# Kernel tuning notes

Hardware: AMD Instinct MI355X
Metric: run time of the kernel (lower is better)

The kernel has to match this reference:

```python
import jax, jax.numpy as jnp
import numpy as np

N = 100000
E = 1600000
D = 128          # in_feat == hidden_size
L = 3            # hidden layers
EPS = 1e-5       # BatchNorm1d eps


def setup_inputs() -> dict:
    key = jax.random.key(0)
    ks = jax.random.split(key, 12)
    x = jax.random.normal(ks[0], (N, D), dtype=jnp.float32)
    edge_index = jax.random.randint(ks[1], (2, E), 0, N, dtype=jnp.int64)
    s = 1.0 / np.sqrt(D)
    # stacked hidden-layer SAGEConv params: lin_l (neighbor), lin_r (root), bias on lin_l
    Wl = jax.random.uniform(ks[2], (L, D, D), jnp.float32, -s, s)
    Wr = jax.random.uniform(ks[3], (L, D, D), jnp.float32, -s, s)
    b = jax.random.uniform(ks[4], (L, D), jnp.float32, -s, s)
    # batchnorm affine params
    gamma = jnp.ones((L, D), jnp.float32)
    beta = jnp.zeros((L, D), jnp.float32)
    # output SAGEConv: D -> 1
    Wl_out = jax.random.uniform(ks[5], (D, 1), jnp.float32, -s, s)
    Wr_out = jax.random.uniform(ks[6], (D, 1), jnp.float32, -s, s)
    b_out = jax.random.uniform(ks[7], (1,), jnp.float32, -s, s)
    return {"x": x, "edge_index": edge_index, "Wl": Wl, "Wr": Wr, "b": b,
            "gamma": gamma, "beta": beta, "Wl_out": Wl_out, "Wr_out": Wr_out,
            "b_out": b_out}


def _sage(x, src, dst, inv_deg, Wl, Wr, b):
    # gather neighbor features along edges, mean-aggregate at destination
    msg_sum = jax.ops.segment_sum(x[src], dst, num_segments=N)   # [N, F]
    mean = msg_sum * inv_deg                                     # 0 for isolated nodes
    return mean @ Wl + x @ Wr + b


def _batchnorm(x, gamma, beta):
    m = jnp.mean(x, axis=0)
    v = jnp.mean((x - m) ** 2, axis=0)  # biased var, as torch BN uses for normalization
    return gamma * (x - m) * jax.lax.rsqrt(v + EPS) + beta


def reference(x, edge_index, Wl, Wr, b, gamma, beta, Wl_out, Wr_out, b_out):
    src, dst = edge_index[0], edge_index[1]
    deg = jax.ops.segment_sum(jnp.ones((E,), x.dtype), dst, num_segments=N)
    inv_deg = jnp.where(deg > 0, 1.0 / jnp.maximum(deg, 1.0), 0.0)[:, None]
    h = x
    for i in range(L):
        h = _sage(h, src, dst, inv_deg, Wl[i], Wr[i], b[i])
        h = jax.nn.relu(h)
        h = _batchnorm(h, gamma[i], beta[i])
    out = _sage(h, src, dst, inv_deg, Wl_out, Wr_out, b_out)
    return jax.nn.sigmoid(out)  # [N, 1]
```

## Files before the change

kernel.cpp:

```cpp
#include <hip/hip_runtime.h>

typedef unsigned short u16;
typedef unsigned int u32;
typedef unsigned long long u64;

#define GN 100000
#define GE 1600000
#define DCAP 64
#define NRANGE 196
#define NBKT (NRANGE * 8)
#define BCAP 1536

typedef __bf16 bf16x8 __attribute__((ext_vector_type(8)));
typedef float f32x4 __attribute__((ext_vector_type(4)));
typedef float f32x2 __attribute__((ext_vector_type(2)));
typedef u32 u32x4 __attribute__((ext_vector_type(4)));
typedef u32 u32x2 __attribute__((ext_vector_type(2)));

__device__ __forceinline__ float bl(u32 u){ return __uint_as_float(u << 16); }
__device__ __forceinline__ float bh(u32 u){ return __uint_as_float(u & 0xffff0000u); }
__device__ __forceinline__ float bfu(u16 v){ return __uint_as_float(((u32)v) << 16); }
__device__ __forceinline__ u16 f2bf(float f){
    u32 u = __float_as_uint(f);
    u32 r = (u + 0x7fffu + ((u >> 16) & 1u)) >> 16;
    return (u16)r;
}
__device__ __forceinline__ u32 pack2(float a, float b){
    return (u32)f2bf(a) | ((u32)f2bf(b) << 16);
}
__device__ __forceinline__ u32 pk8x4(float a, float b, float c, float d){
    u32 p = (u32)__builtin_amdgcn_cvt_pk_fp8_f32(a, b, 0, false);
    p = (u32)__builtin_amdgcn_cvt_pk_fp8_f32(c, d, p, true);
    return p;
}

__global__ void __launch_bounds__(256) k_init(const int* ei, const u32* xraw,
                                              int* cursor, float* colpart, int* flags,
                                              int* bcur){
    int i = blockIdx.x * 256 + threadIdx.x;
    if (i < GN) cursor[i] = 0;
    if (i < NBKT) bcur[i] = 0;
    if (i < 6144) colpart[i] = 0.f;
    int t = threadIdx.x;
    if (blockIdx.x == 0){
        __shared__ int s_any[4];
        int v = 0;
        #pragma unroll
        for (int j = 0; j < 4; ++j){
            int k = t * 4 + j;
            v |= ei[2 * k * 1000 + 1];
        }
        #pragma unroll
        for (int m = 1; m < 64; m <<= 1) v |= __shfl_xor(v, m);
        if ((t & 63) == 0) s_any[t >> 6] = v;
        __syncthreads();
        if (t == 0){
            int any = s_any[0] | s_any[1] | s_any[2] | s_any[3];
            flags[0] = (any == 0) ? 1 : 0;
        }
    }
    if (blockIdx.x == 1){
        __shared__ int s_cnt[4];
        int cnt = 0;
        #pragma unroll
        for (int j = 0; j < 4; ++j){
            int idx = (t * 4 + j) * 6000 + 3;
            u32 u = xraw[idx];
            int e = (u >> 7) & 0xFF;
            cnt += (e >= 100 && e <= 140) ? 1 : 0;
        }
        #pragma unroll
        for (int m = 1; m < 64; m <<= 1) cnt += __shfl_xor(cnt, m);
        if ((t & 63) == 0) s_cnt[t >> 6] = cnt;
        __syncthreads();
        if (t == 0){
            int tot = s_cnt[0] + s_cnt[1] + s_cnt[2] + s_cnt[3];
            flags[1] = (tot > 512) ? 0 : 1;
        }
    }
}

__global__ void __launch_bounds__(256) k_convx(const void* x, const int* flags,
                                               u16* xb, u32* h8){
    int gid = blockIdx.x * 256 + threadIdx.x;
    if (gid >= GN * 16) return;
    float f0,f1,f2,f3,f4,f5,f6,f7;
    if (flags[1]){
        const u32x4* xf = (const u32x4*)x;
        u32x4 a = __builtin_nontemporal_load(xf + gid * 2);
        u32x4 b = __builtin_nontemporal_load(xf + gid * 2 + 1);
        f0 = __uint_as_float(a.x); f1 = __uint_as_float(a.y);
        f2 = __uint_as_float(a.z); f3 = __uint_as_float(a.w);
        f4 = __uint_as_float(b.x); f5 = __uint_as_float(b.y);
        f6 = __uint_as_float(b.z); f7 = __uint_as_float(b.w);
    } else {
        u32x4 g = __builtin_nontemporal_load((const u32x4*)x + gid);
        f0 = bl(g.x); f1 = bh(g.x); f2 = bl(g.y); f3 = bh(g.y);
        f4 = bl(g.z); f5 = bh(g.z); f6 = bl(g.w); f7 = bh(g.w);
    }
    u32x4 o;
    o.x = pack2(f0, f1); o.y = pack2(f2, f3);
    o.z = pack2(f4, f5); o.w = pack2(f6, f7);
    ((u32x4*)xb)[gid] = o;
    u32x2 e = { pk8x4(f0, f1, f2, f3), pk8x4(f4, f5, f6, f7) };
    ((u32x2*)h8)[gid] = e;
}

__global__ void __launch_bounds__(256) k_tofp8(const u16* h, u32* h8){
    int gid = blockIdx.x * 256 + threadIdx.x;
    if (gid >= GN * 16) return;
    u32x4 g = ((const u32x4*)h)[gid];
    u32x2 e = { pk8x4(bl(g.x), bh(g.x), bl(g.y), bh(g.y)),
                pk8x4(bl(g.z), bh(g.z), bl(g.w), bh(g.w)) };
    ((u32x2*)h8)[gid] = e;
}

#define WOFF_WR    49152
#define WOFF_B     98304
#define WOFF_G     98688
#define WOFF_BE    99072
#define WOFF_WLO   99456
#define WOFF_WRO   99584
#define WOFF_BO    99712
#define WTOT       99713
__global__ void __launch_bounds__(256) k_convw(const void* Wl, const void* Wr, const void* b,
                                               const void* g, const void* be, const void* wlo,
                                               const void* wro, const void* bo,
                                               const int* flags, u16* wbuf, float* biasf){
    int i = blockIdx.x * 256 + threadIdx.x;
    if (i >= WTOT) return;
    const void* s; int k;
    if (i < WOFF_B){
        const void* src = (i < WOFF_WR) ? Wl : Wr;
        int r = (i < WOFF_WR) ? i : i - WOFF_WR;
        int layer = r >> 14, L = r & 16383;
        int kk = ((L >> 10) << 3) | (L & 7);
        int cc = (L >> 3) & 127;
        int si = layer * 16384 + kk * 128 + cc;
        float fv = flags[1] ? ((const float*)src)[si] : bfu(((const u16*)src)[si]);
        wbuf[i] = f2bf(fv);
        return;
    }
    if      (i < WOFF_G  ){ s = b;   k = i - WOFF_B; }
    else if (i < WOFF_BE ){ s = g;   k = i - WOFF_G; }
    else if (i < WOFF_WLO){ s = be;  k = i - WOFF_BE; }
    else if (i < WOFF_WRO){ s = wlo; k = i - WOFF_WLO; }
    else if (i < WOFF_BO ){ s = wro; k = i - WOFF_WRO; }
    else                  { s = bo;  k = 0; }
    float fv = flags[1] ? ((const float*)s)[k] : bfu(((const u16*)s)[k]);
    wbuf[i] = f2bf(fv);
    if (i >= WOFF_B && i < WOFF_B + 384) biasf[i - WOFF_B] = fv;
}

__global__ void __launch_bounds__(256) k_fillA(const int* ei, const int* flags,
                                               int* bcur, u64* pairs){
    __shared__ int cnt[256];
    __shared__ int lofs[256];
    __shared__ int gbase[NRANGE];
    __shared__ int wsum[4];
    __shared__ u64 lp[1024];
    int t = threadIdx.x;
    int lane = t & 63, w = t >> 6;
    int res = blockIdx.x & 7;
    int base = blockIdx.x * 1024;
    int is64 = flags[0];
    cnt[t] = 0;
    __syncthreads();
    int myd[4], mys[4], slot[4], myr[4];
    #pragma unroll
    for (int j = 0; j < 4; ++j){
        int e = base + j * 256 + t;
        if (e < GE){
            int d, s;
            if (is64){ d = __builtin_nontemporal_load(ei + 2 * (GE + e));
                       s = __builtin_nontemporal_load(ei + 2 * e); }
            else     { d = __builtin_nontemporal_load(ei + GE + e);
                       s = __builtin_nontemporal_load(ei + e); }
            myd[j] = d; mys[j] = s; myr[j] = d >> 9;
            slot[j] = atomicAdd(&cnt[myr[j]], 1);
        } else myr[j] = -1;
    }
    __syncthreads();
    int v = cnt[t];
    int sv = v;
    #pragma unroll
    for (int d = 1; d < 64; d <<= 1){
        int u = __shfl_up(sv, d);
        if (lane >= d) sv += u;
    }
    if (lane == 63) wsum[w] = sv;
    __syncthreads();
    int prefix = 0;
    #pragma unroll
    for (int j = 0; j < 4; ++j) if (j < w) prefix += wsum[j];
    lofs[t] = sv + prefix - v;
    if (t < NRANGE && cnt[t] > 0)
        gbase[t] = atomicAdd(&bcur[t * 8 + res], cnt[t]);
    __syncthreads();
    #pragma unroll
    for (int j = 0; j < 4; ++j){
        if (myr[j] >= 0)
            lp[lofs[myr[j]] + slot[j]] = ((u64)(u32)myd[j] << 32) | (u32)mys[j];
    }
    __syncthreads();
    int total = GE - base; if (total > 1024) total = 1024;
    for (int i = t; i < total; i += 256){
        u64 pr = lp[i];
        int r = (int)(pr >> 32) >> 9;
        int g = gbase[r] + (i - lofs[r]);
        if (g < BCAP) pairs[((size_t)(r * 8 + res)) * BCAP + g] = pr;
    }
}

__global__ void __launch_bounds__(256) k_fillB(const int* bcur, const u64* pairs,
                                               int* cursor, int* col){
    int range = blockIdx.x % 200;
    int sub   = blockIdx.x / 200;
    if (range >= NRANGE || sub >= 8) return;
    int bkt = range * 8 + sub;
    int n = bcur[bkt]; if (n > BCAP) n = BCAP;
    const u64* P = pairs + (size_t)bkt * BCAP;
    for (int i = threadIdx.x; i < n; i += 256){
        u64 pr = __builtin_nontemporal_load(P + i);
        int s = (int)(u32)pr, d = (int)(pr >> 32);
        int pos = atomicAdd(&cursor[d], 1);
        if (pos < DCAP) col[d * DCAP + pos] = s;
    }
}

__global__ void __launch_bounds__(256, 4) k_aggemm(const u32* h8, const int* deg, const int* col,
                                                   const u16* hin, const u16* Wlp, const u16* Wrp,
                                                   const float* biasf,
                                                   u16* hout, float* colpart){
    __shared__ __align__(16) u16 albuf[4][32][136];
    int t = threadIdx.x;
    int wid = t >> 6, lane = t & 63;
    int grp = lane >> 4, lg = lane & 15;
    int r0w = blockIdx.x * 128 + wid * 32;

    const u32x2* hrow = (const u32x2*)h8;
    #pragma unroll 1
    for (int round = 0; round < 8; ++round){
        int nl = round * 4 + grp;
        int node = r0w + nl;
        float a0=0.f,a1=0.f,a2=0.f,a3=0.f,a4=0.f,a5=0.f,a6=0.f,a7=0.f;
        if (node < GN){
            int d = deg[node];
            int cnt = d < DCAP ? d : DCAP;
            const int* nb = col + node * DCAP;
            int e = 0;
            #define ACC8(v) { \
                f32x2 d0 = __builtin_amdgcn_cvt_pk_f32_fp8((v).x, false); \
                f32x2 d1 = __builtin_amdgcn_cvt_pk_f32_fp8((v).x, true);  \
                f32x2 d2 = __builtin_amdgcn_cvt_pk_f32_fp8((v).y, false); \
                f32x2 d3 = __builtin_amdgcn_cvt_pk_f32_fp8((v).y, true);  \
                a0 += d0.x; a1 += d0.y; a2 += d1.x; a3 += d1.y;           \
                a4 += d2.x; a5 += d2.y; a6 += d3.x; a7 += d3.y; }
            for (; e + 7 < cnt; e += 8){
                u32x2 v0 = hrow[(size_t)nb[e]     * 16 + lg];
                u32x2 v1 = hrow[(size_t)nb[e + 1] * 16 + lg];
                u32x2 v2 = hrow[(size_t)nb[e + 2] * 16 + lg];
                u32x2 v3 = hrow[(size_t)nb[e + 3] * 16 + lg];
                u32x2 v4 = hrow[(size_t)nb[e + 4] * 16 + lg];
                u32x2 v5 = hrow[(size_t)nb[e + 5] * 16 + lg];
                u32x2 v6 = hrow[(size_t)nb[e + 6] * 16 + lg];
                u32x2 v7 = hrow[(size_t)nb[e + 7] * 16 + lg];
                ACC8(v0) ACC8(v1) ACC8(v2) ACC8(v3) ACC8(v4) ACC8(v5) ACC8(v6) ACC8(v7)
            }
            for (; e + 1 < cnt; e += 2){
                u32x2 v0 = hrow[(size_t)nb[e]     * 16 + lg];
                u32x2 v1 = hrow[(size_t)nb[e + 1] * 16 + lg];
                ACC8(v0) ACC8(v1)
            }
            if (e < cnt){
                u32x2 v0 = hrow[(size_t)nb[e] * 16 + lg];
                ACC8(v0)
            }
            #undef ACC8
            float inv = (d > 0) ? 1.f / (float)d : 0.f;
            a0*=inv; a1*=inv; a2*=inv; a3*=inv; a4*=inv; a5*=inv; a6*=inv; a7*=inv;
        }
        u32x4 o;
        o.x = pack2(a0, a1); o.y = pack2(a2, a3);
        o.z = pack2(a4, a5); o.w = pack2(a6, a7);
        *(u32x4*)(&albuf[wid][nl][lg * 8]) = o;
    }

    int quad = grp, l15 = lg;
    f32x4 acc[2][8];
    #pragma unroll
    for (int i = 0; i < 2; i++)
        #pragma unroll
        for (int j = 0; j < 8; j++) acc[i][j] = (f32x4){0.f, 0.f, 0.f, 0.f};

    #pragma unroll
    for (int half = 0; half < 2; ++half){
        const u16* W = half ? Wrp : Wlp;
        #pragma unroll
        for (int s = 0; s < 4; ++s){
            int kk = (s << 5) + (quad << 3);
            union { u32x4 u; bf16x8 v; } fn0, fn1;
            if (half == 0){
                fn0.u = *(const u32x4*)(&albuf[wid][l15][kk]);
                fn1.u = *(const u32x4*)(&albuf[wid][l15 + 16][kk]);
            } else {
                int n0 = r0w + l15, n1 = r0w + 16 + l15;
                fn0.u = (n0 < GN) ? *(const u32x4*)(hin + n0 * 128 + kk) : (u32x4){0,0,0,0};
                fn1.u = (n1 < GN) ? *(const u32x4*)(hin + n1 * 128 + kk) : (u32x4){0,0,0,0};
            }
            int kc = (s << 2) + quad;
            const u32x4* wg = (const u32x4*)W + (kc << 7) + l15;
            #pragma unroll
            for (int cb = 0; cb < 8; ++cb){
                union { u32x4 u; bf16x8 v; } fw;
                fw.u = wg[cb << 4];
                acc[0][cb] = __builtin_amdgcn_mfma_f32_16x16x32_bf16(fn0.v, fw.v, acc[0][cb], 0, 0, 0);
                acc[1][cb] = __builtin_amdgcn_mfma_f32_16x16x32_bf16(fn1.v, fw.v, acc[1][cb], 0, 0, 0);
            }
        }
    }

    __syncthreads();
    float* sst = (float*)albuf;
    sst[t] = 0.f;
    __syncthreads();

    int r0 = r0w;
    float bsv[8];
    #pragma unroll
    for (int cb = 0; cb < 8; cb++) bsv[cb] = biasf[cb * 16 + l15];

    #pragma unroll
    for (int cb = 0; cb < 8; cb++){
        float csum = 0.f, csq = 0.f;
        #pragma unroll
        for (int rb = 0; rb < 2; rb++){
            int rbase = r0 + rb * 16 + quad * 4;
            #pragma unroll
            for (int rr = 0; rr < 4; rr++){
                int row = rbase + rr;
                float v = acc[rb][cb][rr] + bsv[cb];
                v = fmaxf(v, 0.f);
                if (row < GN) hout[row * 128 + cb * 16 + l15] = f2bf(v);
                float vm = (row < GN) ? v : 0.f;
                csum += vm; csq += vm * vm;
            }
        }
        csum += __shfl_xor(csum, 16); csum += __shfl_xor(csum, 32);
        csq  += __shfl_xor(csq, 16);  csq  += __shfl_xor(csq, 32);
        if (quad == 0){
            atomicAdd(&sst[cb * 16 + l15], csum);
            atomicAdd(&sst[128 + cb * 16 + l15], csq);
        }
    }
    __syncthreads();
    atomicAdd(&colpart[(blockIdx.x & 7) * 256 + t], sst[t]);
}

__global__ void __launch_bounds__(256) k_bnf(const float* colpart, const u16* gamma, const u16* beta,
                                             int mode,
                                             const u16* WlN, const u16* WrN, u16* wfd,
                                             const float* bNsrc, float* bNdst,
                                             const u16* wlo, const u16* wro, const u16* bo,
                                             u16* hwl, u16* hwr, float* hb){
    __shared__ float s_sc[128], s_sh[128], s_red[256];
    int t = threadIdx.x, b = blockIdx.x;
    if (t < 128){
        float s = 0.f, q = 0.f;
        #pragma unroll
        for (int j = 0; j < 8; ++j){
            s += colpart[j * 256 + t];
            q += colpart[j * 256 + 128 + t];
        }
        const float invn = 1.f / (float)GN;
        float mean = s * invn;
        float var = fmaxf(q * invn - mean * mean, 0.f);
        float rstd = rsqrtf(var + 1e-5f);
        float g  = bfu(gamma[t]);
        float be = bfu(beta[t]);
        float sc = g * rstd, sh = be - mean * sc;
        s_sc[t] = sc; s_sh[t] = sh;
    }
    __syncthreads();
    if (mode == 0){
        if (b < 64){
            int idx = b * 256 + t;
            int k = ((idx >> 10) << 3) | (idx & 7);
            float sc = s_sc[k];
            wfd[idx]         = f2bf(sc * bfu(WlN[idx]));
            wfd[16384 + idx] = f2bf(sc * bfu(WrN[idx]));
        } else if (t < 128){
            float acc = bNsrc[t];
            for (int k = 0; k < 128; ++k){
                int L = ((k >> 3) << 10) + (t << 3) + (k & 7);
                acc += s_sh[k] * (bfu(WlN[L]) + bfu(WrN[L]));
            }
            bNdst[t] = acc;
        }
    } else if (b == 64){
        float contrib = 0.f;
        if (t < 128){
            float wl = bfu(wlo[t]), wr = bfu(wro[t]);
            hwl[t] = f2bf(s_sc[t] * wl);
            hwr[t] = f2bf(s_sc[t] * wr);
            contrib = s_sh[t] * (wl + wr);
        }
        s_red[t] = contrib;
        __syncthreads();
        for (int off = 128; off >= 1; off >>= 1){
            if (t < off) s_red[t] += s_red[t + off];
            __syncthreads();
        }
        if (t == 0) hb[0] = s_red[0] + bfu(bo[0]);
    }
}

__global__ void __launch_bounds__(256) k_dot(const u16* h, const u16* wl, const u16* wr,
                                             float* y, float* r){
    int node = (blockIdx.x * 256 + threadIdx.x) >> 6;
    int lane = threadIdx.x & 63;
    if (node >= GN) return;
    u32 hv  = ((const u32*)h)[node * 64 + lane];
    u32 wlv = ((const u32*)wl)[lane];
    u32 wrv = ((const u32*)wr)[lane];
    float hlo = bl(hv), hhi = bh(hv);
    float ya = hlo * bl(wlv) + hhi * bh(wlv);
    float ra = hlo * bl(wrv) + hhi * bh(wrv);
    #pragma unroll
    for (int m = 1; m < 64; m <<= 1){ ya += __shfl_xor(ya, m); ra += __shfl_xor(ra, m); }
    if (lane == 0){ y[node] = ya; r[node] = ra; }
}

__global__ void __launch_bounds__(256) k_out(const float* y, const float* r, const int* deg,
                                             const int* col, const float* hb,
                                             const int* flags, void* out){
    int n = blockIdx.x * 256 + threadIdx.x;
    if (n >= GN) return;
    int d = deg[n];
    int cnt = d < DCAP ? d : DCAP;
    const int* nb = col + n * DCAP;
    float s = 0.f;
    for (int e = 0; e < cnt; ++e) s += y[nb[e]];
    float inv = (d > 0) ? 1.f / (float)d : 0.f;
    float z = inv * s + r[n] + hb[0];
    float sg = 1.f / (1.f + __expf(-z));
    if (flags[1]) ((float*)out)[n] = sg;
    else          ((u16*)out)[n] = f2bf(sg);
}

extern "C" void kernel_launch(void* const* d_in, const int* in_sizes, int n_in,
                              void* d_out, int out_size, void* d_ws, size_t ws_size,
                              hipStream_t stream) {
    const void* x     = d_in[0];
    const int*  ei    = (const int*)d_in[1];
    const void* Wl    = d_in[2];
    const void* Wr    = d_in[3];
    const void* bias  = d_in[4];
    const void* gamma = d_in[5];
    const void* beta  = d_in[6];
    const void* wlout = d_in[7];
    const void* wrout = d_in[8];
    const void* bout  = d_in[9];

    char* p = (char*)d_ws;
    auto take = [&](size_t b){ void* q = (void*)p; p += (b + 255) & ~(size_t)255; return q; };
    int*   cursor = (int*)  take((size_t)GN * 4);
    int*   flags  = (int*)  take(256);
    int*   bcur   = (int*)  take((size_t)NBKT * 4);
    float* colpart= (float*)take(6144 * 4);
    float* biasf  = (float*)take(384 * 4);
    float* bf2    = (float*)take(128 * 4);
    float* bf3    = (float*)take(128 * 4);
    float* hb     = (float*)take(256);
    u16*   wf2    = (u16*)  take(32768 * 2);
    u16*   wf3    = (u16*)  take(32768 * 2);
    u16*   hwl    = (u16*)  take(128 * 2);
    u16*   hwr    = (u16*)  take(128 * 2);
    float* yv     = (float*)take((size_t)GN * 4);
    float* rv     = (float*)take((size_t)GN * 4);
    int*   col    = (int*)  take((size_t)GN * DCAP * 4);
    u16*   xb     = (u16*)  take((size_t)GN * 128 * 2);
    u16*   scrap  = (u16*)  take((size_t)GN * 128 * 2);
    u16*   hbuf   = (u16*)  take((size_t)GN * 128 * 2);
    u32*   h8     = (u32*)  take((size_t)GN * 128);
    u16*   wbuf   = (u16*)  take((size_t)WTOT * 2);

    u64* pairs = (u64*)scrap;

    const int NB_N = (GN + 255) / 256;
    const int NB_W = (GN + 3) / 4;
    const int NB_G = (GN + 127) / 128;
    const int NB_M = (GN * 16 + 255) / 256;
    const int NB_C = (WTOT + 255) / 256;
    const int NB_A = (GE + 1023) / 1024;

    k_init <<<NB_N, 256, 0, stream>>>(ei, (const u32*)x, cursor, colpart, flags, bcur);
    k_convx<<<NB_M, 256, 0, stream>>>(x, flags, xb, h8);
    k_convw<<<NB_C, 256, 0, stream>>>(Wl, Wr, bias, gamma, beta, wlout, wrout, bout, flags, wbuf, biasf);
    k_fillA<<<NB_A, 256, 0, stream>>>(ei, flags, bcur, pairs);
    k_fillB<<<1600, 256, 0, stream>>>(bcur, pairs, cursor, col);

    const u16* hin = xb;
    for (int i = 0; i < 3; ++i){
        const u16* Wlp; const u16* Wrp; const float* bfi;
        if (i == 0){ Wlp = wbuf;     Wrp = wbuf + WOFF_WR; bfi = biasf; }
        else if (i == 1){ Wlp = wf2; Wrp = wf2 + 16384;    bfi = bf2; }
        else { Wlp = wf3;            Wrp = wf3 + 16384;    bfi = bf3; }
        u16* wfd = (i == 0) ? wf2 : wf3;
        float* bNdst = (i == 0) ? bf2 : bf3;
        int nx = (i < 2) ? (i + 1) : 0;
        k_aggemm<<<NB_G, 256, 0, stream>>>(h8, cursor, col, hin, Wlp, Wrp, bfi, hbuf,
                                           colpart + i * 2048);
        k_bnf  <<<65, 256, 0, stream>>>(colpart + i * 2048,
            wbuf + WOFF_G + i * 128, wbuf + WOFF_BE + i * 128, (i == 2) ? 1 : 0,
            wbuf + nx * 16384, wbuf + WOFF_WR + nx * 16384, wfd,
            biasf + nx * 128, bNdst,
            wbuf + WOFF_WLO, wbuf + WOFF_WRO, wbuf + WOFF_BO, hwl, hwr, hb);
        if (i < 2) k_tofp8<<<NB_M, 256, 0, stream>>>(hbuf, h8);
        hin = hbuf;
    }
    k_dot<<<NB_W, 256, 0, stream>>>(hbuf, hwl, hwr, yv, rv);
    k_out<<<NB_N, 256, 0, stream>>>(yv, rv, cursor, col, hb, flags, d_out);
}
```

Measured before the change: 457.5 us.

## Split fused aggregate+GEMM kernel into separate gather and MFMA GEMM kernels

The fused per-layer kernel, which gathered fp8 neighbor rows into LDS and then ran the bf16 MFMA GEMM, is split into two kernels. A small 64-thread-block gather kernel writes bf16 mean rows to a global buffer, and a separate GEMM kernel reads them back. This aims to improve latency hiding and occupancy for the irregular gather by decoupling it from the register-heavy GEMM. The cost is an extra round trip of about 25.6 MB per layer through global memory, plus one more kernel launch per layer.

```diff
diff --git a/kernel.cpp b/kernel.cpp
--- a/kernel.cpp
+++ b/kernel.cpp
@@ -228,65 +228,68 @@
     }
 }
 
-__global__ void __launch_bounds__(256, 4) k_aggemm(const u32* h8, const int* deg, const int* col,
-                                                   const u16* hin, const u16* Wlp, const u16* Wrp,
-                                                   const float* biasf,
-                                                   u16* hout, float* colpart){
-    __shared__ __align__(16) u16 albuf[4][32][136];
+__global__ void __launch_bounds__(64) k_agg(const u32* h8, const int* deg, const int* col,
+                                            u16* amean){
+    int lane = threadIdx.x;
+    int grp = lane >> 4;
+    int lg  = lane & 15;
+    int node = blockIdx.x * 4 + grp;
+    if (node >= GN) return;
+    int d = deg[node];
+    int cnt = d < DCAP ? d : DCAP;
+    const int* nb = col + node * DCAP;
+    const u32x2* hrow = (const u32x2*)h8;
+    float a0=0.f,a1=0.f,a2=0.f,a3=0.f,a4=0.f,a5=0.f,a6=0.f,a7=0.f;
+    int e = 0;
+    #define ACC8(v) { \
+        f32x2 d0 = __builtin_amdgcn_cvt_pk_f32_fp8((v).x, false); \
+        f32x2 d1 = __builtin_amdgcn_cvt_pk_f32_fp8((v).x, true);  \
+        f32x2 d2 = __builtin_amdgcn_cvt_pk_f32_fp8((v).y, false); \
+        f32x2 d3 = __builtin_amdgcn_cvt_pk_f32_fp8((v).y, true);  \
+        a0 += d0.x; a1 += d0.y; a2 += d1.x; a3 += d1.y;           \
+        a4 += d2.x; a5 += d2.y; a6 += d3.x; a7 += d3.y; }
+    for (; e + 7 < cnt; e += 8){
+        u32x2 v0 = hrow[(size_t)nb[e]     * 16 + lg];
+        u32x2 v1 = hrow[(size_t)nb[e + 1] * 16 + lg];
+        u32x2 v2 = hrow[(size_t)nb[e + 2] * 16 + lg];
+        u32x2 v3 = hrow[(size_t)nb[e + 3] * 16 + lg];
+        u32x2 v4 = hrow[(size_t)nb[e + 4] * 16 + lg];
+        u32x2 v5 = hrow[(size_t)nb[e + 5] * 16 + lg];
+        u32x2 v6 = hrow[(size_t)nb[e + 6] * 16 + lg];
+        u32x2 v7 = hrow[(size_t)nb[e + 7] * 16 + lg];
+        ACC8(v0) ACC8(v1) ACC8(v2) ACC8(v3) ACC8(v4) ACC8(v5) ACC8(v6) ACC8(v7)
+    }
+    for (; e + 1 < cnt; e += 2){
+        u32x2 v0 = hrow[(size_t)nb[e]     * 16 + lg];
+        u32x2 v1 = hrow[(size_t)nb[e + 1] * 16 + lg];
+        ACC8(v0) ACC8(v1)
+    }
+    if (e < cnt){
+        u32x2 v0 = hrow[(size_t)nb[e] * 16 + lg];
+        ACC8(v0)
+    }
+    #undef ACC8
+    float inv = (d > 0) ? 1.f / (float)d : 0.f;
+    u32x4 o;
+    o.x = pack2(a0 * inv, a1 * inv);
+    o.y = pack2(a2 * inv, a3 * inv);
+    o.z = pack2(a4 * inv, a5 * inv);
+    o.w = pack2(a6 * inv, a7 * inv);
+    ((u32x4*)amean)[(size_t)node * 16 + lg] = o;
+}
+
+__global__ void __launch_bounds__(256, 4) k_gemm(const u16* amean, const u16* hin,
+                                                 const u16* Wlp, const u16* Wrp,
+                                                 const float* biasf,
+                                                 u16* hout, float* colpart){
+    __shared__ float sst[256];
     int t = threadIdx.x;
     int wid = t >> 6, lane = t & 63;
-    int grp = lane >> 4, lg = lane & 15;
-    int r0w = blockIdx.x * 128 + wid * 32;
-
-    const u32x2* hrow = (const u32x2*)h8;
-    #pragma unroll 1
-    for (int round = 0; round < 8; ++round){
-        int nl = round * 4 + grp;
-        int node = r0w + nl;
-        float a0=0.f,a1=0.f,a2=0.f,a3=0.f,a4=0.f,a5=0.f,a6=0.f,a7=0.f;
-        if (node < GN){
-            int d = deg[node];
-            int cnt = d < DCAP ? d : DCAP;
-            const int* nb = col + node * DCAP;
-            int e = 0;
-            #define ACC8(v) { \
-                f32x2 d0 = __builtin_amdgcn_cvt_pk_f32_fp8((v).x, false); \
-                f32x2 d1 = __builtin_amdgcn_cvt_pk_f32_fp8((v).x, true);  \
-                f32x2 d2 = __builtin_amdgcn_cvt_pk_f32_fp8((v).y, false); \
-                f32x2 d3 = __builtin_amdgcn_cvt_pk_f32_fp8((v).y, true);  \
-                a0 += d0.x; a1 += d0.y; a2 += d1.x; a3 += d1.y;           \
-                a4 += d2.x; a5 += d2.y; a6 += d3.x; a7 += d3.y; }
-            for (; e + 7 < cnt; e += 8){
-                u32x2 v0 = hrow[(size_t)nb[e]     * 16 + lg];
-                u32x2 v1 = hrow[(size_t)nb[e + 1] * 16 + lg];
-                u32x2 v2 = hrow[(size_t)nb[e + 2] * 16 + lg];
-                u32x2 v3 = hrow[(size_t)nb[e + 3] * 16 + lg];
-                u32x2 v4 = hrow[(size_t)nb[e + 4] * 16 + lg];
-                u32x2 v5 = hrow[(size_t)nb[e + 5] * 16 + lg];
-                u32x2 v6 = hrow[(size_t)nb[e + 6] * 16 + lg];
-                u32x2 v7 = hrow[(size_t)nb[e + 7] * 16 + lg];
-                ACC8(v0) ACC8(v1) ACC8(v2) ACC8(v3) ACC8(v4) ACC8(v5) ACC8(v6) ACC8(v7)
-            }
-            for (; e + 1 < cnt; e += 2){
-                u32x2 v0 = hrow[(size_t)nb[e]     * 16 + lg];
-                u32x2 v1 = hrow[(size_t)nb[e + 1] * 16 + lg];
-                ACC8(v0) ACC8(v1)
-            }
-            if (e < cnt){
-                u32x2 v0 = hrow[(size_t)nb[e] * 16 + lg];
-                ACC8(v0)
-            }
-            #undef ACC8
-            float inv = (d > 0) ? 1.f / (float)d : 0.f;
-            a0*=inv; a1*=inv; a2*=inv; a3*=inv; a4*=inv; a5*=inv; a6*=inv; a7*=inv;
-        }
-        u32x4 o;
-        o.x = pack2(a0, a1); o.y = pack2(a2, a3);
-        o.z = pack2(a4, a5); o.w = pack2(a6, a7);
-        *(u32x4*)(&albuf[wid][nl][lg * 8]) = o;
-    }
-
-    int quad = grp, l15 = lg;
+    int quad = lane >> 4, l15 = lane & 15;
+    int r0 = blockIdx.x * 128 + wid * 32;
+    int node0 = r0 + l15, node1 = r0 + 16 + l15;
+    sst[t] = 0.f;
+
     f32x4 acc[2][8];
     #pragma unroll
     for (int i = 0; i < 2; i++)
@@ -295,37 +298,27 @@
 
     #pragma unroll
     for (int half = 0; half < 2; ++half){
-        const u16* W = half ? Wrp : Wlp;
+        const u16* A = half ? hin : amean;
+        const u32x4* Wg = (const u32x4*)(half ? Wrp : Wlp);
         #pragma unroll
         for (int s = 0; s < 4; ++s){
             int kk = (s << 5) + (quad << 3);
-            union { u32x4 u; bf16x8 v; } fn0, fn1;
-            if (half == 0){
-                fn0.u = *(const u32x4*)(&albuf[wid][l15][kk]);
-                fn1.u = *(const u32x4*)(&albuf[wid][l15 + 16][kk]);
-            } else {
-                int n0 = r0w + l15, n1 = r0w + 16 + l15;
-                fn0.u = (n0 < GN) ? *(const u32x4*)(hin + n0 * 128 + kk) : (u32x4){0,0,0,0};
-                fn1.u = (n1 < GN) ? *(const u32x4*)(hin + n1 * 128 + kk) : (u32x4){0,0,0,0};
-            }
+            union { u32x4 u; bf16x8 v; } fa0, fa1;
+            fa0.u = (node0 < GN) ? *(const u32x4*)(A + node0 * 128 + kk) : (u32x4){0,0,0,0};
+            fa1.u = (node1 < GN) ? *(const u32x4*)(A + node1 * 128 + kk) : (u32x4){0,0,0,0};
             int kc = (s << 2) + quad;
-            const u32x4* wg = (const u32x4*)W + (kc << 7) + l15;
+            const u32x4* wg = Wg + (kc << 7) + l15;
             #pragma unroll
             for (int cb = 0; cb < 8; ++cb){
                 union { u32x4 u; bf16x8 v; } fw;
                 fw.u = wg[cb << 4];
-                acc[0][cb] = __builtin_amdgcn_mfma_f32_16x16x32_bf16(fn0.v, fw.v, acc[0][cb], 0, 0, 0);
-                acc[1][cb] = __builtin_amdgcn_mfma_f32_16x16x32_bf16(fn1.v, fw.v, acc[1][cb], 0, 0, 0);
+                acc[0][cb] = __builtin_amdgcn_mfma_f32_16x16x32_bf16(fa0.v, fw.v, acc[0][cb], 0, 0, 0);
+                acc[1][cb] = __builtin_amdgcn_mfma_f32_16x16x32_bf16(fa1.v, fw.v, acc[1][cb], 0, 0, 0);
             }
         }
     }
-
-    __syncthreads();
-    float* sst = (float*)albuf;
-    sst[t] = 0.f;
-    __syncthreads();
-
-    int r0 = r0w;
+    __syncthreads();
+
     float bsv[8];
     #pragma unroll
     for (int cb = 0; cb < 8; cb++) bsv[cb] = biasf[cb * 16 + l15];
@@ -480,14 +473,15 @@
     float* rv     = (float*)take((size_t)GN * 4);
     int*   col    = (int*)  take((size_t)GN * DCAP * 4);
     u16*   xb     = (u16*)  take((size_t)GN * 128 * 2);
-    u16*   scrap  = (u16*)  take((size_t)GN * 128 * 2);
+    u16*   amean  = (u16*)  take((size_t)GN * 128 * 2);
     u16*   hbuf   = (u16*)  take((size_t)GN * 128 * 2);
     u32*   h8     = (u32*)  take((size_t)GN * 128);
     u16*   wbuf   = (u16*)  take((size_t)WTOT * 2);
 
-    u64* pairs = (u64*)scrap;
+    u64* pairs = (u64*)amean;
 
     const int NB_N = (GN + 255) / 256;
+    const int NB_A4 = (GN + 3) / 4;
     const int NB_W = (GN + 3) / 4;
     const int NB_G = (GN + 127) / 128;
     const int NB_M = (GN * 16 + 255) / 256;
@@ -509,9 +503,10 @@
         u16* wfd = (i == 0) ? wf2 : wf3;
         float* bNdst = (i == 0) ? bf2 : bf3;
         int nx = (i < 2) ? (i + 1) : 0;
-        k_aggemm<<<NB_G, 256, 0, stream>>>(h8, cursor, col, hin, Wlp, Wrp, bfi, hbuf,
-                                           colpart + i * 2048);
-        k_bnf  <<<65, 256, 0, stream>>>(colpart + i * 2048,
+        k_agg <<<NB_A4, 64, 0, stream>>>(h8, cursor, col, amean);
+        k_gemm<<<NB_G, 256, 0, stream>>>(amean, hin, Wlp, Wrp, bfi, hbuf,
+                                         colpart + i * 2048);
+        k_bnf <<<65, 256, 0, stream>>>(colpart + i * 2048,
             wbuf + WOFF_G + i * 128, wbuf + WOFF_BE + i * 128, (i == 2) ? 1 : 0,
             wbuf + nx * 16384, wbuf + WOFF_WR + nx * 16384, wfd,
             biasf + nx * 128, bNdst,
```

Result: no change. 462.5 us (+1.1%).
